# Kernel optimization log

Measured on AMD Instinct MI355X. Metric: run time of the kernel, lower is better.

Reference implementation:

```python
import math
import jax, jax.numpy as jnp
import numpy as np

TOPK = 13
NUM_CLASSES = 80
ALPHA = 1.0
BETA = 6.0
EPS = 1e-9


def _ciou(b1, b2, eps=1e-7):
    """CIoU between broadcastable xyxy boxes b1 (gt) and b2 (pred); matches bbox_iou(xywh=False, CIoU=True)."""
    b1x1, b1y1, b1x2, b1y2 = (b1[..., 0], b1[..., 1], b1[..., 2], b1[..., 3])
    b2x1, b2y1, b2x2, b2y2 = (b2[..., 0], b2[..., 1], b2[..., 2], b2[..., 3])
    w1, h1 = b1x2 - b1x1, b1y2 - b1y1 + eps
    w2, h2 = b2x2 - b2x1, b2y2 - b2y1 + eps
    inter = (jnp.clip(jnp.minimum(b1x2, b2x2) - jnp.maximum(b1x1, b2x1), 0.0, None)
             * jnp.clip(jnp.minimum(b1y2, b2y2) - jnp.maximum(b1y1, b2y1), 0.0, None))
    union = w1 * h1 + w2 * h2 - inter + eps
    iou = inter / union
    cw = jnp.maximum(b1x2, b2x2) - jnp.minimum(b1x1, b2x1)
    ch = jnp.maximum(b1y2, b2y2) - jnp.minimum(b1y1, b2y1)
    c2 = cw * cw + ch * ch + eps
    rho2 = ((b2x1 + b2x2 - b1x1 - b1x2) ** 2 + (b2y1 + b2y2 - b1y1 - b1y2) ** 2) / 4.0
    v = (4.0 / math.pi ** 2) * (jnp.arctan(w2 / h2) - jnp.arctan(w1 / h1)) ** 2
    alpha = jax.lax.stop_gradient(v / (v - iou + (1.0 + eps)))  # torch.no_grad() block
    return iou - (rho2 / c2 + v * alpha)


def setup_inputs() -> dict:
    key = jax.random.key(0)
    ks = jax.random.split(key, 7)
    bs, M, nc, img = 16, 128, NUM_CLASSES, 640
    # YOLO anchor points for 640x640, strides 8/16/32 -> 8400 points (pixel coords)
    pts = []
    for s in (8, 16, 32):
        n = img // s
        g = (jnp.arange(n, dtype=jnp.float32) + 0.5) * s
        yv, xv = jnp.meshgrid(g, g, indexing='ij')
        pts.append(jnp.stack([xv, yv], -1).reshape(-1, 2))
    anc_points = jnp.concatenate(pts, 0)  # (8400, 2)
    na = anc_points.shape[0]
    pd_scores = jax.random.uniform(ks[0], (bs, na, nc), dtype=jnp.float32)
    # predicted boxes: xyxy around each anchor point
    cxy = anc_points[None] + jax.random.normal(ks[1], (bs, na, 2)) * 4.0
    wh = jax.random.uniform(ks[2], (bs, na, 2), minval=4.0, maxval=96.0)
    pd_bboxes = jnp.concatenate([cxy - wh / 2, cxy + wh / 2], -1)
    # gt boxes: xyxy in image coords
    g_cxy = jax.random.uniform(ks[3], (bs, M, 2), minval=0.0, maxval=640.0)
    g_wh = jax.random.uniform(ks[4], (bs, M, 2), minval=16.0, maxval=200.0)
    gt_bboxes = jnp.concatenate([g_cxy - g_wh / 2, g_cxy + g_wh / 2], -1)
    gt_labels = jax.random.randint(ks[5], (bs, M, 1), 0, nc, dtype=jnp.int32)
    mask_gt = (jax.random.uniform(ks[6], (bs, M, 1)) < 0.8).astype(jnp.float32)
    return {'pd_scores': pd_scores, 'pd_bboxes': pd_bboxes, 'anc_points': anc_points,
            'gt_labels': gt_labels, 'gt_bboxes': gt_bboxes, 'mask_gt': mask_gt}


def reference(pd_scores, pd_bboxes, anc_points, gt_labels, gt_bboxes, mask_gt):
    bs, na, nc = pd_scores.shape
    M = gt_bboxes.shape[1]
    dt = pd_scores.dtype

    # ---- select_candidates_in_gts: anchor center strictly inside gt box ----
    lt = gt_bboxes[:, :, None, :2]   # (bs,M,1,2)
    rb = gt_bboxes[:, :, None, 2:]   # (bs,M,1,2)
    anc = anc_points[None, None]     # (1,1,na,2)
    d_min = jnp.minimum((anc - lt).min(-1), (rb - anc).min(-1))  # (bs,M,na)
    mask_in_gts = (d_min > EPS).astype(dt)

    # ---- get_box_metrics (dense, masked where torch left zeros) ----
    mask = (mask_in_gts * mask_gt) > 0  # (bs,M,na) bool
    lbl = gt_labels[..., 0]             # (bs,M) int
    # pd_scores[b, :, label] -> (bs,M,na)
    gathered = pd_scores[jnp.arange(bs)[:, None], :, lbl]
    bbox_scores = jnp.where(mask, gathered, 0.0)
    ciou = _ciou(gt_bboxes[:, :, None, :], pd_bboxes[:, None, :, :])  # (bs,M,na)
    overlaps = jnp.where(mask, jnp.clip(ciou, 0.0, None), 0.0)
    align_metric = bbox_scores ** ALPHA * overlaps ** BETA

    # ---- select_topk_candidates ----
    _, topk_idxs = jax.lax.top_k(align_metric, TOPK)            # (bs,M,TOPK)
    topk_idxs = jnp.where(mask_gt > 0, topk_idxs, 0)            # masked_fill_(~topk_mask, 0)
    row_off = (jnp.arange(bs * M, dtype=topk_idxs.dtype) * na).reshape(bs, M, 1)
    counts = (jnp.zeros(bs * M * na, jnp.int32)
              .at[(topk_idxs + row_off).ravel()].add(1)
              .reshape(bs, M, na))
    mask_topk = jnp.where(counts > 1, 0, counts).astype(dt)     # drop anchors hit >1 time per gt

    mask_pos = mask_topk * mask_in_gts * mask_gt                # (bs,M,na)

    # ---- select_highest_overlaps: resolve anchors claimed by multiple gts ----
    fg_mask = mask_pos.sum(1)                                   # (bs,na)
    mask_multi = fg_mask[:, None, :] > 1                        # (bs,1,na)
    max_ov_idx = overlaps.argmax(1)                             # (bs,na)
    is_max = jax.nn.one_hot(max_ov_idx, M, dtype=dt).transpose(0, 2, 1)  # (bs,M,na)
    mask_pos = jnp.where(mask_multi, is_max, mask_pos)
    fg_mask = mask_pos.sum(1)
    target_gt_idx = mask_pos.argmax(1)                          # (bs,na)

    # ---- get_targets ----
    flat_idx = target_gt_idx + jnp.arange(bs, dtype=target_gt_idx.dtype)[:, None] * M
    target_labels = jnp.clip(gt_labels.reshape(-1)[flat_idx], 0, None)     # (bs,na)
    target_bboxes = gt_bboxes.reshape(-1, 4)[flat_idx]                     # (bs,na,4)
    target_scores = jax.nn.one_hot(target_labels, nc, dtype=dt)
    target_scores = jnp.where(fg_mask[..., None] > 0, target_scores, 0.0)

    # ---- normalization of target scores ----
    am = align_metric * mask_pos
    pos_am = am.max(-1, keepdims=True)                          # (bs,M,1)
    pos_ov = (overlaps * mask_pos).max(-1, keepdims=True)       # (bs,M,1)
    norm = (am * pos_ov / (pos_am + EPS)).max(1)[..., None]     # (bs,na,1)
    target_scores = target_scores * norm

    return (target_labels, target_bboxes, target_scores, fg_mask > 0, target_gt_idx)
```

## Files before the change

kernel.cpp:

```cpp
#include <hip/hip_runtime.h>
#include <math.h>

constexpr int BS = 16;
constexpr int NA = 8400;
constexpr int NC = 80;
constexpr int MG = 128;
constexpr int TK = 13;
constexpr int NCAND = 1536;

constexpr int OFF_LBL = 0;
constexpr int OFF_BB  = OFF_LBL + BS * NA;
constexpr int OFF_SC  = OFF_BB  + BS * NA * 4;
constexpr int OFF_FG  = OFF_SC  + BS * NA * NC;
constexpr int OFF_TG  = OFF_FG  + BS * NA;

__device__ __forceinline__ float ciou_pre(float gx, float gy, float gz, float gw,
                                          float px, float py, float pz, float pw,
                                          float dat) {
    const float eps = 1e-7f;
    float w1 = gz - gx, h1 = gw - gy + eps;
    float w2 = pz - px, h2 = pw - py + eps;
    float iw = fmaxf(fminf(gz, pz) - fmaxf(gx, px), 0.f);
    float ih = fmaxf(fminf(gw, pw) - fmaxf(gy, py), 0.f);
    float inter = iw * ih;
    float uni = w1 * h1 + w2 * h2 - inter + eps;
    float iou = inter / uni;
    float cw = fmaxf(gz, pz) - fminf(gx, px);
    float ch = fmaxf(gw, pw) - fminf(gy, py);
    float c2 = cw * cw + ch * ch + eps;
    float dx = px + pz - gx - gz;
    float dy = py + pw - gy - gw;
    float rho2 = (dx * dx + dy * dy) * 0.25f;
    float v = 0.4052847345693511f * dat * dat;
    float alpha = v / (v - iou + (1.f + eps));
    return iou - (rho2 / c2 + v * alpha);
}

__device__ __forceinline__ bool inside_gt(float ax, float ay,
                                          float gx, float gy, float gz, float gw) {
    float d = fminf(fminf(ax - gx, ay - gy), fminf(gz - ax, gw - ay));
    return d > 1e-9f;
}

__device__ __forceinline__ void anchor_xy(int a, float& ax, float& ay) {
    if (a < 6400)      { int iy = a / 80;        int ix = a - iy * 80;           ax = (ix + 0.5f) * 8.f;  ay = (iy + 0.5f) * 8.f; }
    else if (a < 8000) { int r = a - 6400; int iy = r / 40; int ix = r - iy * 40; ax = (ix + 0.5f) * 16.f; ay = (iy + 0.5f) * 16.f; }
    else               { int r = a - 8000; int iy = r / 20; int ix = r - iy * 20; ax = (ix + 0.5f) * 32.f; ay = (iy + 0.5f) * 32.f; }
}

__global__ __launch_bounds__(128) void k_topk(
    const float* __restrict__ pd_scores, const float* __restrict__ pd_bboxes,
    const int* __restrict__ gt_labels, const float* __restrict__ gt_bboxes,
    const float* __restrict__ mask_gt,
    int* __restrict__ fg_cnt, int* __restrict__ fg_m,
    float* __restrict__ at_g_tbl)
{
    __shared__ float cv[NCAND];
    __shared__ int   ca[NCAND];
    __shared__ int   s_cnt;
    __shared__ unsigned s_pm;
    __shared__ float s_wv[2];
    __shared__ int   s_wk[2];

    int bm = blockIdx.x;
    if (mask_gt[bm] <= 0.f) return;
    int b = bm >> 7;
    int m = bm & (MG - 1);
    int tid = threadIdx.x;

    if (tid == 0) { s_cnt = 0; s_pm = 0u; }
    __syncthreads();

    const float4 g = *reinterpret_cast<const float4*>(gt_bboxes + bm * 4);
    const int lbl = gt_labels[bm];
    const float* pbb = pd_bboxes + (size_t)b * NA * 4;
    const float* psc = pd_scores + (size_t)b * NA * NC;
    const float at_g = atanf((g.z - g.x) / (g.w - g.y + 1e-7f));
    if (tid == 0) at_g_tbl[bm] = at_g;

    auto do_level = [&](float s, int n, int base) {
        int xlo = max(0, (int)floorf(g.x / s - 0.5f) - 1);
        int xhi = min(n - 1, (int)ceilf(g.z / s - 0.5f) + 1);
        int ylo = max(0, (int)floorf(g.y / s - 0.5f) - 1);
        int yhi = min(n - 1, (int)ceilf(g.w / s - 0.5f) + 1);
        int w = xhi - xlo + 1, h = yhi - ylo + 1;
        if (w <= 0 || h <= 0) return;
        int cnt = w * h;
        for (int idx = tid; idx < cnt; idx += 128) {
            int iy = ylo + idx / w;
            int ix = xlo + idx - (idx / w) * w;
            float ax = (ix + 0.5f) * s;
            float ay = (iy + 0.5f) * s;
            if (!inside_gt(ax, ay, g.x, g.y, g.z, g.w)) continue;
            int a = base + iy * n + ix;
            float4 p = *reinterpret_cast<const float4*>(pbb + (size_t)a * 4);
            float dat = atanf((p.z - p.x) / (p.w - p.y + 1e-7f)) - at_g;
            float ov = fmaxf(ciou_pre(g.x, g.y, g.z, g.w, p.x, p.y, p.z, p.w, dat), 0.f);
            float sc = psc[(size_t)a * NC + lbl];
            float ov2 = ov * ov;
            float al = sc * ov2 * ov2 * ov2;
            if (al > 0.f) {
                int slot = atomicAdd(&s_cnt, 1);
                if (slot < NCAND) { cv[slot] = al; ca[slot] = a; }
                if (a < 32) atomicOr(&s_pm, 1u << a);
            }
        }
    };
    do_level(8.f, 80, 0);
    do_level(16.f, 40, 6400);
    do_level(32.f, 20, 8000);
    __syncthreads();

    int npos = min(s_cnt, NCAND);
    int rounds = min(npos, TK);
    int* fgc = fg_cnt + b * NA;
    int* fgm = fg_m + b * NA;

    for (int k = 0; k < rounds; ++k) {
        float bv = -1.f; int bk = 0x7fffffff;
        for (int p = tid; p < npos; p += 128) {
            float v = cv[p];
            int key = (ca[p] << 11) | p;
            if (v > bv || (v == bv && key < bk)) { bv = v; bk = key; }
        }
        #pragma unroll
        for (int off = 32; off > 0; off >>= 1) {
            float v2 = __shfl_down(bv, off);
            int   k2 = __shfl_down(bk, off);
            if (v2 > bv || (v2 == bv && k2 < bk)) { bv = v2; bk = k2; }
        }
        int wid = tid >> 6;
        if ((tid & 63) == 0) { s_wv[wid] = bv; s_wk[wid] = bk; }
        __syncthreads();
        if (tid == 0) {
            if (s_wv[1] > bv || (s_wv[1] == bv && s_wk[1] < bk)) { bv = s_wv[1]; bk = s_wk[1]; }
            int slot = bk & 2047;
            int a = bk >> 11;
            cv[slot] = -1.f;
            atomicAdd(&fgc[a], 1);
            fgm[a] = m;
        }
        __syncthreads();
    }

    if (tid == 0) {
        int need = TK - rounds;
        unsigned pm = s_pm;
        for (int idx = 0; idx < 32 && need > 0; ++idx) {
            if (!((pm >> idx) & 1u)) {
                float ax = (idx + 0.5f) * 8.f, ay = 4.f;
                if (inside_gt(ax, ay, g.x, g.y, g.z, g.w)) {
                    atomicAdd(&fgc[idx], 1);
                    fgm[idx] = m;
                }
                --need;
            }
        }
    }
}

__global__ __launch_bounds__(256) void k_assign(
    const float* __restrict__ pd_scores, const float* __restrict__ pd_bboxes,
    const int* __restrict__ gt_labels, const float* __restrict__ gt_bboxes,
    const float* __restrict__ mask_gt, const float* __restrict__ at_g_tbl,
    const int* __restrict__ fg_cnt, const int* __restrict__ fg_m,
    float* __restrict__ out, float* __restrict__ am_ws,
    int* __restrict__ gi_ws, int* __restrict__ lbl_ws,
    unsigned* __restrict__ pos_am, unsigned* __restrict__ pos_ov)
{
    int i = blockIdx.x * 256 + threadIdx.x;
    int cnt = fg_cnt[i];
    int b = i / NA, a = i - b * NA;
    int gbase = b * MG;

    int t = 0;
    float bov = -1.f;
    bool multi = cnt > 1;
    if (multi) {
        float ax, ay; anchor_xy(a, ax, ay);
        float4 p = *reinterpret_cast<const float4*>(pd_bboxes + (size_t)i * 4);
        float at_p = atanf((p.z - p.x) / (p.w - p.y + 1e-7f));
        for (int mm = 0; mm < MG; ++mm) {
            int gi = gbase + mm;
            float ov = 0.f;
            if (mask_gt[gi] > 0.f) {
                float4 gg = *reinterpret_cast<const float4*>(gt_bboxes + gi * 4);
                if (inside_gt(ax, ay, gg.x, gg.y, gg.z, gg.w)) {
                    float dat = at_p - at_g_tbl[gi];
                    ov = fmaxf(ciou_pre(gg.x, gg.y, gg.z, gg.w, p.x, p.y, p.z, p.w, dat), 0.f);
                }
            }
            if (ov > bov) { bov = ov; t = mm; }
        }
    } else if (cnt == 1) {
        t = fg_m[i];
    }

    int gi = gbase + t;
    float4 g = *reinterpret_cast<const float4*>(gt_bboxes + gi * 4);
    int lraw = gt_labels[gi];
    int lbl = max(lraw, 0);

    float am = 0.f, ovv = 0.f;
    if (multi) {
        if (bov > 0.f) {
            float sc = pd_scores[(size_t)i * NC + lraw];
            float o2 = bov * bov;
            am = sc * o2 * o2 * o2;
            ovv = bov;
        }
    } else if (cnt == 1) {
        if (mask_gt[gi] > 0.f) {
            float ax, ay; anchor_xy(a, ax, ay);
            if (inside_gt(ax, ay, g.x, g.y, g.z, g.w)) {
                float4 p = *reinterpret_cast<const float4*>(pd_bboxes + (size_t)i * 4);
                float dat = atanf((p.z - p.x) / (p.w - p.y + 1e-7f)) - at_g_tbl[gi];
                float ov = fmaxf(ciou_pre(g.x, g.y, g.z, g.w, p.x, p.y, p.z, p.w, dat), 0.f);
                float sc = pd_scores[(size_t)i * NC + lraw];
                float ov2 = ov * ov;
                am = sc * ov2 * ov2 * ov2;
                ovv = ov;
            }
        }
    }

    if (cnt > 0) {
        atomicMax(&pos_am[gi], __float_as_uint(am));
        atomicMax(&pos_ov[gi], __float_as_uint(ovv));
        am_ws[i] = am; gi_ws[i] = gi; lbl_ws[i] = lbl;
    } else {
        gi_ws[i] = -1;
    }

    out[OFF_LBL + i] = (float)lbl;
    reinterpret_cast<float4*>(out + OFF_BB)[i] = g;
    out[OFF_FG + i] = cnt ? 1.f : 0.f;
    out[OFF_TG + i] = (float)t;
}

__global__ __launch_bounds__(256) void k_scores(
    const float* __restrict__ am_ws, const int* __restrict__ gi_ws,
    const int* __restrict__ lbl_ws,
    const unsigned* __restrict__ pos_am, const unsigned* __restrict__ pos_ov,
    float* __restrict__ out_scores)
{
    constexpr int NQ = NC / 4;
    int idx = blockIdx.x * 256 + threadIdx.x;
    int i = idx / NQ;
    int q = idx - i * NQ;
    float4 v = {0.f, 0.f, 0.f, 0.f};
    int gi = gi_ws[i];
    if (gi >= 0) {
        int lbl = lbl_ws[i];
        if ((lbl >> 2) == q) {
            float norm = am_ws[i] * __uint_as_float(pos_ov[gi]) /
                         (__uint_as_float(pos_am[gi]) + 1e-9f);
            reinterpret_cast<float*>(&v)[lbl & 3] = norm;
        }
    }
    reinterpret_cast<float4*>(out_scores)[idx] = v;
}

extern "C" void kernel_launch(void* const* d_in, const int* in_sizes, int n_in,
                              void* d_out, int out_size, void* d_ws, size_t ws_size,
                              hipStream_t stream) {
    const float* pd_scores = (const float*)d_in[0];
    const float* pd_bboxes = (const float*)d_in[1];
    const int*   gt_labels = (const int*)d_in[3];
    const float* gt_bboxes = (const float*)d_in[4];
    const float* mask_gt   = (const float*)d_in[5];
    float* out = (float*)d_out;

    unsigned char* w = (unsigned char*)d_ws;
    size_t off = 0;
    int*      fg_cnt   = (int*)(w + off);      off += (size_t)BS * NA * 4;
    unsigned* pos_am   = (unsigned*)(w + off); off += (size_t)BS * MG * 4;
    unsigned* pos_ov   = (unsigned*)(w + off); off += (size_t)BS * MG * 4;
    size_t zero_bytes = off;
    int*      fg_m     = (int*)(w + off);      off += (size_t)BS * NA * 4;
    float*    am_ws    = (float*)(w + off);    off += (size_t)BS * NA * 4;
    int*      gi_ws    = (int*)(w + off);      off += (size_t)BS * NA * 4;
    int*      lbl_ws   = (int*)(w + off);      off += (size_t)BS * NA * 4;
    float*    at_g_tbl = (float*)(w + off);    off += (size_t)BS * MG * 4;

    hipMemsetAsync(w, 0, zero_bytes, stream);

    k_topk<<<BS * MG, 128, 0, stream>>>(pd_scores, pd_bboxes, gt_labels,
                                        gt_bboxes, mask_gt, fg_cnt, fg_m,
                                        at_g_tbl);

    int nA = BS * NA;
    k_assign<<<nA / 256, 256, 0, stream>>>(
        pd_scores, pd_bboxes, gt_labels, gt_bboxes, mask_gt, at_g_tbl,
        fg_cnt, fg_m, out, am_ws, gi_ws, lbl_ws, pos_am, pos_ov);

    k_scores<<<nA * (NC / 4) / 256, 256, 0, stream>>>(
        am_ws, gi_ws, lbl_ws, pos_am, pos_ov, out + OFF_SC);
}
```

Before: 183.4 us.

## Use single-wave topk blocks and wave-cooperative argmax for multi-assigned anchors

k_topk now runs one 64-lane wavefront per gt box instead of two. That removes the shared-memory cross-wave merge and one barrier per top-k round, at the cost of fewer threads scanning the candidate window. In k_assign, anchors claimed by several gts are handled cooperatively: the whole wave evaluates the 128 CIoUs for each such anchor, two per lane, then takes the argmax with a shuffle reduction. This replaces a serial 128-iteration loop per thread that caused divergence, and adds ballot/shuffle overhead for each multi-assigned anchor.

```diff
diff --git a/kernel.cpp b/kernel.cpp
--- a/kernel.cpp
+++ b/kernel.cpp
@@ -48,7 +48,7 @@
     else               { int r = a - 8000; int iy = r / 20; int ix = r - iy * 20; ax = (ix + 0.5f) * 32.f; ay = (iy + 0.5f) * 32.f; }
 }
 
-__global__ __launch_bounds__(128) void k_topk(
+__global__ __launch_bounds__(64) void k_topk(
     const float* __restrict__ pd_scores, const float* __restrict__ pd_bboxes,
     const int* __restrict__ gt_labels, const float* __restrict__ gt_bboxes,
     const float* __restrict__ mask_gt,
@@ -59,8 +59,6 @@
     __shared__ int   ca[NCAND];
     __shared__ int   s_cnt;
     __shared__ unsigned s_pm;
-    __shared__ float s_wv[2];
-    __shared__ int   s_wk[2];
 
     int bm = blockIdx.x;
     if (mask_gt[bm] <= 0.f) return;
@@ -86,7 +84,7 @@
         int w = xhi - xlo + 1, h = yhi - ylo + 1;
         if (w <= 0 || h <= 0) return;
         int cnt = w * h;
-        for (int idx = tid; idx < cnt; idx += 128) {
+        for (int idx = tid; idx < cnt; idx += 64) {
             int iy = ylo + idx / w;
             int ix = xlo + idx - (idx / w) * w;
             float ax = (ix + 0.5f) * s;
@@ -118,7 +116,7 @@
 
     for (int k = 0; k < rounds; ++k) {
         float bv = -1.f; int bk = 0x7fffffff;
-        for (int p = tid; p < npos; p += 128) {
+        for (int p = tid; p < npos; p += 64) {
             float v = cv[p];
             int key = (ca[p] << 11) | p;
             if (v > bv || (v == bv && key < bk)) { bv = v; bk = key; }
@@ -129,11 +127,7 @@
             int   k2 = __shfl_down(bk, off);
             if (v2 > bv || (v2 == bv && k2 < bk)) { bv = v2; bk = k2; }
         }
-        int wid = tid >> 6;
-        if ((tid & 63) == 0) { s_wv[wid] = bv; s_wk[wid] = bk; }
-        __syncthreads();
         if (tid == 0) {
-            if (s_wv[1] > bv || (s_wv[1] == bv && s_wk[1] < bk)) { bv = s_wv[1]; bk = s_wk[1]; }
             int slot = bk & 2047;
             int a = bk >> 11;
             cv[slot] = -1.f;
@@ -168,20 +162,29 @@
     int* __restrict__ gi_ws, int* __restrict__ lbl_ws,
     unsigned* __restrict__ pos_am, unsigned* __restrict__ pos_ov)
 {
-    int i = blockIdx.x * 256 + threadIdx.x;
+    int tid = threadIdx.x;
+    int i = blockIdx.x * 256 + tid;
     int cnt = fg_cnt[i];
     int b = i / NA, a = i - b * NA;
     int gbase = b * MG;
+    int lane = tid & 63;
+    bool multi = cnt > 1;
 
     int t = 0;
-    float bov = -1.f;
-    bool multi = cnt > 1;
-    if (multi) {
-        float ax, ay; anchor_xy(a, ax, ay);
-        float4 p = *reinterpret_cast<const float4*>(pd_bboxes + (size_t)i * 4);
+    float bovm = -1.f;
+
+    unsigned long long mk = __ballot(multi);
+    while (mk) {
+        int l = __ffsll((long long)mk) - 1; mk &= mk - 1ull;
+        int ii = __shfl(i, l);
+        int bb = ii / NA, aa = ii - bb * NA;
+        int gb = bb * MG;
+        float ax, ay; anchor_xy(aa, ax, ay);
+        float4 p = *reinterpret_cast<const float4*>(pd_bboxes + (size_t)ii * 4);
         float at_p = atanf((p.z - p.x) / (p.w - p.y + 1e-7f));
-        for (int mm = 0; mm < MG; ++mm) {
-            int gi = gbase + mm;
+
+        auto ovm = [&](int mm) -> float {
+            int gi = gb + mm;
             float ov = 0.f;
             if (mask_gt[gi] > 0.f) {
                 float4 gg = *reinterpret_cast<const float4*>(gt_bboxes + gi * 4);
@@ -190,11 +193,25 @@
                     ov = fmaxf(ciou_pre(gg.x, gg.y, gg.z, gg.w, p.x, p.y, p.z, p.w, dat), 0.f);
                 }
             }
-            if (ov > bov) { bov = ov; t = mm; }
-        }
-    } else if (cnt == 1) {
-        t = fg_m[i];
-    }
+            return ov;
+        };
+        float ov0 = ovm(lane);
+        float ov1 = ovm(lane + 64);
+        float bov; int bmx;
+        if (ov1 > ov0) { bov = ov1; bmx = lane + 64; }
+        else           { bov = ov0; bmx = lane; }
+        #pragma unroll
+        for (int off = 32; off > 0; off >>= 1) {
+            float v2 = __shfl_down(bov, off);
+            int   m2 = __shfl_down(bmx, off);
+            if (v2 > bov || (v2 == bov && m2 < bmx)) { bov = v2; bmx = m2; }
+        }
+        bov = __shfl(bov, 0);
+        bmx = __shfl(bmx, 0);
+        if (lane == l) { t = bmx; bovm = bov; }
+    }
+
+    if (!multi && cnt == 1) t = fg_m[i];
 
     int gi = gbase + t;
     float4 g = *reinterpret_cast<const float4*>(gt_bboxes + gi * 4);
@@ -203,11 +220,11 @@
 
     float am = 0.f, ovv = 0.f;
     if (multi) {
-        if (bov > 0.f) {
+        if (bovm > 0.f) {
             float sc = pd_scores[(size_t)i * NC + lraw];
-            float o2 = bov * bov;
+            float o2 = bovm * bovm;
             am = sc * o2 * o2 * o2;
-            ovv = bov;
+            ovv = bovm;
         }
     } else if (cnt == 1) {
         if (mask_gt[gi] > 0.f) {
@@ -285,9 +302,9 @@
 
     hipMemsetAsync(w, 0, zero_bytes, stream);
 
-    k_topk<<<BS * MG, 128, 0, stream>>>(pd_scores, pd_bboxes, gt_labels,
-                                        gt_bboxes, mask_gt, fg_cnt, fg_m,
-                                        at_g_tbl);
+    k_topk<<<BS * MG, 64, 0, stream>>>(pd_scores, pd_bboxes, gt_labels,
+                                       gt_bboxes, mask_gt, fg_cnt, fg_m,
+                                       at_g_tbl);
 
     int nA = BS * NA;
     k_assign<<<nA / 256, 256, 0, stream>>>(
```

Measured after the change: 163.5 us. 10.9% less time.
